# Optimization experiments

Measured on AMD Instinct MI355X. Metric: run time of the kernel, lower is better.

Reference implementation:

```python
import jax, jax.numpy as jnp
import numpy as np

D_MODEL = 1024
N_HEADS = 16
HEAD_DIM = D_MODEL // N_HEADS
THETA = 10000.0


def _rope_tables(seq_len, d_k, dtype):
    pos = jnp.arange(seq_len, dtype=jnp.float32)
    dim = jnp.arange(0, d_k, 2, dtype=jnp.float32)
    inv_freq = 1.0 / (THETA ** (dim / d_k))  # [d_k//2]
    angle = pos[:, None] * inv_freq[None, :]  # [seq, d_k//2]
    return jnp.cos(angle).astype(dtype), jnp.sin(angle).astype(dtype)


def _apply_rope(x, cos, sin):
    # x: [B, H, S, d_k]; cos/sin: [S, d_k//2] (interleaved-pair rotation)
    x1 = x[..., ::2]
    x2 = x[..., 1::2]
    r1 = x1 * cos - x2 * sin
    r2 = x1 * sin + x2 * cos
    out = jnp.stack([r1, r2], axis=-1)  # [..., d_k//2, 2]
    return out.reshape(x.shape)


def setup_inputs() -> dict:
    key = jax.random.key(0)
    ks = jax.random.split(key, 5)
    B, S, D = 4, 2048, D_MODEL
    std = np.sqrt(2.0 / (D + D)).astype(np.float32)
    x = jax.random.normal(ks[0], (B, S, D), dtype=jnp.float32)
    wq = jax.random.normal(ks[1], (D, D), dtype=jnp.float32) * std
    wk = jax.random.normal(ks[2], (D, D), dtype=jnp.float32) * std
    wv = jax.random.normal(ks[3], (D, D), dtype=jnp.float32) * std
    wo = jax.random.normal(ks[4], (D, D), dtype=jnp.float32) * std
    return {"x": x, "wq": wq, "wk": wk, "wv": wv, "wo": wo}


def reference(x, wq, wk, wv, wo):
    B, S, D = x.shape
    H, dk = N_HEADS, HEAD_DIM
    # projections (weight stored [d_out, d_in])
    q = jnp.einsum('oi,bsi->bso', wq, x)
    k = jnp.einsum('oi,bsi->bso', wk, x)
    v = jnp.einsum('oi,bsi->bso', wv, x)
    # split heads -> [B, H, S, dk]
    q = q.reshape(B, S, H, dk).transpose(0, 2, 1, 3)
    k = k.reshape(B, S, H, dk).transpose(0, 2, 1, 3)
    v = v.reshape(B, S, H, dk).transpose(0, 2, 1, 3)
    cos, sin = _rope_tables(S, dk, x.dtype)
    q = _apply_rope(q, cos, sin)
    k = _apply_rope(k, cos, sin)
    scale = 1.0 / np.sqrt(dk)
    logits = jnp.einsum('bhqd,bhkd->bhqk', q, k) * scale
    causal = jnp.tril(jnp.ones((S, S), dtype=bool))
    logits = jnp.where(causal, logits, -jnp.inf)
    probs = jax.nn.softmax(logits, axis=-1)
    ctx = jnp.einsum('bhqk,bhkd->bhqd', probs, v)
    ctx = ctx.transpose(0, 2, 1, 3).reshape(B, S, D)
    return jnp.einsum('oi,bsi->bso', wo, ctx)
```

## Files before the change

### kernel.cpp

```cpp
#include <hip/hip_runtime.h>
#include <hip/hip_bf16.h>
#include <cstdint>
#include <cstddef>


typedef __bf16 bf16;
typedef __bf16 bf16x2 __attribute__((ext_vector_type(2)));
typedef __bf16 bf16x4 __attribute__((ext_vector_type(4)));
typedef __bf16 bf16x8 __attribute__((ext_vector_type(8)));
typedef float  f32x4  __attribute__((ext_vector_type(4)));

#define SEQ 2048
#define NH  16
#define DM  1024
#define MFMA16 __builtin_amdgcn_mfma_f32_16x16x32_bf16

__device__ __forceinline__ void async16(bf16* lds, const bf16* g) {
  __builtin_amdgcn_global_load_lds(
      (__attribute__((address_space(1))) void*)(g),
      (__attribute__((address_space(3))) void*)(lds), 16, 0, 0);
}

__global__ void cvt_all(const float* __restrict__ x,
                        const float* __restrict__ w0, const float* __restrict__ w1,
                        const float* __restrict__ w2, const float* __restrict__ w3,
                        bf16* __restrict__ xb, bf16* __restrict__ wb) {
  int i = blockIdx.x * blockDim.x + threadIdx.x;
  float4 f;
  bf16x4* dst;
  if (i < 2097152) {
    f = ((const float4*)x)[i];
    dst = (bf16x4*)xb + i;
  } else {
    int k = i - 2097152;
    int sel = k >> 18, j = k & 262143;
    const float* src = sel == 0 ? w0 : sel == 1 ? w1 : sel == 2 ? w2 : w3;
    f = ((const float4*)src)[j];
    dst = (bf16x4*)wb + k;
  }
  bf16x4 o;
  o.x = (bf16)f.x; o.y = (bf16)f.y; o.z = (bf16)f.z; o.w = (bf16)f.w;
  *dst = o;
}


__global__ void __launch_bounds__(256)
gemm_out(const bf16* __restrict__ A, const bf16* __restrict__ B,
         float* __restrict__ C, int M, int N, int K) {
  __shared__ bf16 As[2][128 * 32];
  __shared__ bf16 Bs[2][128 * 32];
  const int tid  = threadIdx.x;
  const int lane = tid & 63;
  const int w    = tid >> 6;
  const int l15  = lane & 15, g = lane >> 4;
  const int wr   = w >> 1, wc = w & 1;
  const long bm = (long)blockIdx.x * 128, bn = (long)blockIdx.y * 128;

  f32x4 acc[4][4] = {};

  const int r0 = tid >> 2;
  const int c0 = (tid & 3) << 3;
  const bf16* aB = A + (bm + r0) * K + c0;
  const bf16* bB = B + (bn + r0) * K + c0;

  async16(&As[0][(size_t)tid * 8],        aB);
  async16(&As[0][2048 + (size_t)tid * 8], aB + (size_t)64 * K);
  async16(&Bs[0][(size_t)tid * 8],        bB);
  async16(&Bs[0][2048 + (size_t)tid * 8], bB + (size_t)64 * K);

  const int nkt = K >> 5;
  for (int kt = 0; kt < nkt; ++kt) {
    const int cur = kt & 1, nxt = cur ^ 1;
    __syncthreads();
    if (kt + 1 < nkt) {
      const bf16* ap = aB + (kt + 1) * 32;
      const bf16* bp = bB + (kt + 1) * 32;
      async16(&As[nxt][(size_t)tid * 8],        ap);
      async16(&As[nxt][2048 + (size_t)tid * 8], ap + (size_t)64 * K);
      async16(&Bs[nxt][(size_t)tid * 8],        bp);
      async16(&Bs[nxt][2048 + (size_t)tid * 8], bp + (size_t)64 * K);
    }
    bf16x8 af[4], bfr[4];
#pragma unroll
    for (int mf = 0; mf < 4; ++mf)
      af[mf] = *(const bf16x8*)&As[cur][(wr * 64 + mf * 16 + l15) * 32 + g * 8];
#pragma unroll
    for (int nf = 0; nf < 4; ++nf)
      bfr[nf] = *(const bf16x8*)&Bs[cur][(wc * 64 + nf * 16 + l15) * 32 + g * 8];
#pragma unroll
    for (int mf = 0; mf < 4; ++mf)
#pragma unroll
      for (int nf = 0; nf < 4; ++nf)
        acc[mf][nf] = MFMA16(af[mf], bfr[nf], acc[mf][nf], 0, 0, 0);
  }

#pragma unroll
  for (int mf = 0; mf < 4; ++mf)
#pragma unroll
    for (int nf = 0; nf < 4; ++nf)
#pragma unroll
      for (int r = 0; r < 4; ++r) {
        long m = bm + wr * 64 + mf * 16 + g * 4 + r;
        long n = bn + wc * 64 + nf * 16 + l15;
        C[m * N + n] = acc[mf][nf][r];
      }
}

__global__ void __launch_bounds__(256)
gemm_qkv(const bf16* __restrict__ A, const bf16* __restrict__ Wqkv,
         bf16* __restrict__ Qo, bf16* __restrict__ Ko, bf16* __restrict__ Vto,
         int M, int K) {
  __shared__ bf16 As[2][128 * 32];
  __shared__ bf16 Bs[2][128 * 32];
  const int tid  = threadIdx.x;
  const int lane = tid & 63;
  const int w    = tid >> 6;
  const int l15  = lane & 15, g = lane >> 4;
  const int wr   = w >> 1, wc = w & 1;
  const long bm  = (long)blockIdx.x * 128;
  const long bnG = (long)blockIdx.y * 128;
  const int region = blockIdx.y >> 3;
  const long bn  = (long)(blockIdx.y & 7) * 128;

  f32x4 acc[4][4] = {};

  const int r0 = tid >> 2;
  const int c0 = (tid & 3) << 3;
  const bf16* aB = A + (bm + r0) * K + c0;
  const bf16* bB = Wqkv + (bnG + r0) * K + c0;

  async16(&As[0][(size_t)tid * 8],        aB);
  async16(&As[0][2048 + (size_t)tid * 8], aB + (size_t)64 * K);
  async16(&Bs[0][(size_t)tid * 8],        bB);
  async16(&Bs[0][2048 + (size_t)tid * 8], bB + (size_t)64 * K);

  const int nkt = K >> 5;
  for (int kt = 0; kt < nkt; ++kt) {
    const int cur = kt & 1, nxt = cur ^ 1;
    __syncthreads();
    if (kt + 1 < nkt) {
      const bf16* ap = aB + (kt + 1) * 32;
      const bf16* bp = bB + (kt + 1) * 32;
      async16(&As[nxt][(size_t)tid * 8],        ap);
      async16(&As[nxt][2048 + (size_t)tid * 8], ap + (size_t)64 * K);
      async16(&Bs[nxt][(size_t)tid * 8],        bp);
      async16(&Bs[nxt][2048 + (size_t)tid * 8], bp + (size_t)64 * K);
    }
    bf16x8 af[4], bfr[4];
#pragma unroll
    for (int mf = 0; mf < 4; ++mf)
      af[mf] = *(const bf16x8*)&As[cur][(wr * 64 + mf * 16 + l15) * 32 + g * 8];
#pragma unroll
    for (int nf = 0; nf < 4; ++nf)
      bfr[nf] = *(const bf16x8*)&Bs[cur][(wc * 64 + nf * 16 + l15) * 32 + g * 8];
#pragma unroll
    for (int mf = 0; mf < 4; ++mf)
#pragma unroll
      for (int nf = 0; nf < 4; ++nf)
        acc[mf][nf] = MFMA16(af[mf], bfr[nf], acc[mf][nf], 0, 0, 0);
  }

  if (region < 2) {
    bf16* C = region ? Ko : Qo;
    const float qscale = region ? 1.0f : 0.125f;
#pragma unroll
    for (int nf = 0; nf < 4; ++nf) {
      const int d = nf * 16 + l15;
      const float inv = __expf((float)(d >> 1) * -0.2878231366242558f);
#pragma unroll
      for (int mf = 0; mf < 4; ++mf)
#pragma unroll
        for (int r = 0; r < 4; ++r) {
          long m = bm + wr * 64 + mf * 16 + g * 4 + r;
          long n = bn + wc * 64 + nf * 16 + l15;
          float ang = (float)(int)(m & 2047) * inv;
          float sn, cn;
          __sincosf(ang, &sn, &cn);
          float mine  = acc[mf][nf][r];
          float other = __shfl_xor(mine, 1);
          float res = (d & 1) ? (other * sn + mine * cn)
                              : (mine * cn - other * sn);
          C[m * DM + n] = (bf16)(res * qscale);
        }
    }
  } else {
#pragma unroll
    for (int mf = 0; mf < 4; ++mf)
#pragma unroll
      for (int nf = 0; nf < 4; ++nf) {
        long s0 = bm + wr * 64 + mf * 16 + g * 4;
        long b  = s0 >> 11;
        long s  = s0 & 2047;
        long n  = bn + wc * 64 + nf * 16 + l15;
        long h  = n >> 6, d = n & 63;
        bf16x4 v;
#pragma unroll
        for (int r = 0; r < 4; ++r) v[r] = (bf16)acc[mf][nf][r];
        *(bf16x4*)&Vto[(((b * NH + h) * 64 + d) << 11) + s] = v;
      }
  }
}

__global__ void __launch_bounds__(256, 2)
attn_kernel(const bf16* __restrict__ Q, const bf16* __restrict__ Kg,
            const bf16* __restrict__ Vt, bf16* __restrict__ ctx) {
  __shared__ bf16 Ks[2][64 * 64];
  __shared__ bf16 Vs[2][64 * 64];
  __shared__ bf16 Ps[4 * 2048];
  const int tid  = threadIdx.x;
  const int lane = tid & 63, w = tid >> 6;
  const int l15  = lane & 15, g = lane >> 4;
  const int bid  = (int)blockIdx.x;
  const int qts  = 15 - (bid >> 6);
  const int bh   = bid & 63;
  const int b  = bh >> 4, h = bh & 15;
  const int qw = qts * 128 + w * 32;
  const int ktmax = 2 * qts + 1;

  bf16x8 qf[2][2];
#pragma unroll
  for (int qg = 0; qg < 2; ++qg) {
    const bf16* qp = Q + ((size_t)(b * SEQ + qw + qg * 16 + l15)) * DM + h * 64 + g * 8;
    qf[qg][0] = *(const bf16x8*)qp;
    qf[qg][1] = *(const bf16x8*)(qp + 32);
  }

  f32x4 o[2][4] = {};
  float l_run[2] = {0.f, 0.f};

  const int srow = tid >> 3, scc = tid & 7;
  const int swc  = 8 * (scc ^ (srow & 7));
  const bf16* kb0 = Kg + ((size_t)(b * SEQ + srow)) * DM + h * 64 + swc;
  const bf16* vb0 = Vt + ((size_t)(bh * 64 + srow)) * SEQ + swc;
  bf16* Pw = &Ps[w * 2048];

  async16(&Ks[0][(size_t)tid * 8],        kb0);
  async16(&Ks[0][2048 + (size_t)tid * 8], kb0 + (size_t)32 * DM);
  async16(&Vs[0][(size_t)tid * 8],        vb0);
  async16(&Vs[0][2048 + (size_t)tid * 8], vb0 + (size_t)32 * SEQ);

  for (int kt = 0; kt <= ktmax; ++kt) {
    const int kv0 = kt * 64;
    const int cur = kt & 1, nxt = cur ^ 1;
    __syncthreads();
    if (kt < ktmax) {
      const bf16* kp = kb0 + (size_t)(kt + 1) * 64 * DM;
      const bf16* vp = vb0 + (size_t)(kt + 1) * 64;
      async16(&Ks[nxt][(size_t)tid * 8],        kp);
      async16(&Ks[nxt][2048 + (size_t)tid * 8], kp + (size_t)32 * DM);
      async16(&Vs[nxt][(size_t)tid * 8],        vp);
      async16(&Vs[nxt][2048 + (size_t)tid * 8], vp + (size_t)32 * SEQ);
    }

    if (kv0 > qw + 31) continue;

    f32x4 sa[2][4] = {};
    __builtin_amdgcn_s_setprio(1);
#pragma unroll
    for (int kk = 0; kk < 2; ++kk)
#pragma unroll
      for (int mf = 0; mf < 4; ++mf) {
        const int row = mf * 16 + l15;
        bf16x8 kf = *(const bf16x8*)&Ks[cur][row * 64 + 8 * ((kk * 4 + g) ^ (row & 7))];
        sa[0][mf] = MFMA16(kf, qf[0][kk], sa[0][mf], 0, 0, 0);
        sa[1][mf] = MFMA16(kf, qf[1][kk], sa[1][mf], 0, 0, 0);
      }
    __builtin_amdgcn_s_setprio(0);

#pragma unroll
    for (int j = 0; j < 2; ++j) {
      const int qg = j;
      float p[16];
#pragma unroll
      for (int mf = 0; mf < 4; ++mf)
#pragma unroll
        for (int r = 0; r < 4; ++r) p[mf * 4 + r] = sa[j][mf][r];
      if (kv0 + 63 > qw + qg * 16) {
        const int qidx = qw + qg * 16 + l15;
#pragma unroll
        for (int mf = 0; mf < 4; ++mf)
#pragma unroll
          for (int r = 0; r < 4; ++r)
            if (kv0 + mf * 16 + g * 4 + r > qidx) p[mf * 4 + r] = -1e30f;
      }
      float ts = 0.f;
#pragma unroll
      for (int i = 0; i < 16; ++i) { p[i] = __expf(p[i] - 8.0f); ts += p[i]; }
      l_run[qg] += ts;
#pragma unroll
      for (int mf = 0; mf < 4; ++mf) {
        bf16x4 pv;
#pragma unroll
        for (int r = 0; r < 4; ++r) pv[r] = (bf16)p[mf * 4 + r];
        const int cc = mf * 2 + (g >> 1);
        *(bf16x4*)&Pw[j * 1024 + l15 * 64 + 8 * (cc ^ (l15 & 7)) + (g & 1) * 4] = pv;
      }
    }

    __builtin_amdgcn_s_setprio(1);
#pragma unroll
    for (int kk = 0; kk < 2; ++kk) {
      const int pc = 8 * ((kk * 4 + g) ^ (l15 & 7));
      bf16x8 pa0 = *(const bf16x8*)&Pw[l15 * 64 + pc];
      bf16x8 pa1 = *(const bf16x8*)&Pw[1024 + l15 * 64 + pc];
#pragma unroll
      for (int nf = 0; nf < 4; ++nf) {
        const int vrow = nf * 16 + l15;
        bf16x8 vf = *(const bf16x8*)&Vs[cur][vrow * 64 + 8 * ((kk * 4 + g) ^ (vrow & 7))];
        o[0][nf] = MFMA16(pa0, vf, o[0][nf], 0, 0, 0);
        o[1][nf] = MFMA16(pa1, vf, o[1][nf], 0, 0, 0);
      }
    }
    __builtin_amdgcn_s_setprio(0);
  }

#pragma unroll
  for (int qg = 0; qg < 2; ++qg) {
    float ts = l_run[qg];
    ts += __shfl_xor(ts, 16);
    ts += __shfl_xor(ts, 32);
    float lr[4];
#pragma unroll
    for (int r = 0; r < 4; ++r) lr[r] = 1.0f / __shfl(ts, g * 4 + r);
#pragma unroll
    for (int nf = 0; nf < 4; ++nf)
#pragma unroll
      for (int r = 0; r < 4; ++r) {
        size_t off = ((size_t)(b * SEQ + qw + qg * 16 + g * 4 + r)) * DM + h * 64 + nf * 16 + l15;
        ctx[off] = (bf16)(o[qg][nf][r] * lr[r]);
      }
  }
}

extern "C" void kernel_launch(void* const* d_in, const int* in_sizes, int n_in,
                              void* d_out, int out_size, void* d_ws, size_t ws_size,
                              hipStream_t stream) {
  const float* x  = (const float*)d_in[0];
  const float* wq = (const float*)d_in[1];
  const float* wk = (const float*)d_in[2];
  const float* wv = (const float*)d_in[3];
  const float* wo = (const float*)d_in[4];
  float* out = (float*)d_out;
  char* ws = (char*)d_ws;

  bf16* xb  = (bf16*)(ws);
  bf16* Qb  = (bf16*)(ws + ((size_t)16 << 20));
  bf16* Kb  = (bf16*)(ws + ((size_t)32 << 20));
  bf16* Vt  = (bf16*)(ws + ((size_t)48 << 20));
  bf16* wqb = (bf16*)(ws + ((size_t)64 << 20));
  bf16* wob = (bf16*)(ws + ((size_t)70 << 20));

  cvt_all<<<12288, 256, 0, stream>>>(x, wq, wk, wv, wo, xb, wqb);

  gemm_qkv<<<dim3(64, 24), 256, 0, stream>>>(xb, wqb, Qb, Kb, Vt, 8192, 1024);

  attn_kernel<<<1024, 256, 0, stream>>>(Qb, Kb, Vt, xb );

  gemm_out<<<dim3(64, 8), 256, 0, stream>>>(xb, wob, out, 8192, 1024, 1024);
}
```

Before: 171.4 us.

## Move RoPE out of QKV GEMM epilogue into attention Q load and separate K pass

Removes the per-element sincos/shuffle RoPE epilogue from the QKV projection GEMM so Q and K are stored raw. Q rotation and the 1/sqrt(dk) scale are now applied when the attention kernel loads its Q fragments. K rotation runs in a new standalone elementwise kernel with vectorized 8-wide accesses. The aim is a lighter GEMM epilogue, paid for by an extra launch plus a read and write of all of K, and by bf16 rounding before rotation.

```diff
diff --git a/kernel.cpp b/kernel.cpp
--- a/kernel.cpp
+++ b/kernel.cpp
@@ -162,27 +162,16 @@
 
   if (region < 2) {
     bf16* C = region ? Ko : Qo;
-    const float qscale = region ? 1.0f : 0.125f;
-#pragma unroll
-    for (int nf = 0; nf < 4; ++nf) {
-      const int d = nf * 16 + l15;
-      const float inv = __expf((float)(d >> 1) * -0.2878231366242558f);
-#pragma unroll
-      for (int mf = 0; mf < 4; ++mf)
+#pragma unroll
+    for (int mf = 0; mf < 4; ++mf)
+#pragma unroll
+      for (int nf = 0; nf < 4; ++nf)
 #pragma unroll
         for (int r = 0; r < 4; ++r) {
           long m = bm + wr * 64 + mf * 16 + g * 4 + r;
           long n = bn + wc * 64 + nf * 16 + l15;
-          float ang = (float)(int)(m & 2047) * inv;
-          float sn, cn;
-          __sincosf(ang, &sn, &cn);
-          float mine  = acc[mf][nf][r];
-          float other = __shfl_xor(mine, 1);
-          float res = (d & 1) ? (other * sn + mine * cn)
-                              : (mine * cn - other * sn);
-          C[m * DM + n] = (bf16)(res * qscale);
+          C[m * DM + n] = (bf16)acc[mf][nf][r];
         }
-    }
   } else {
 #pragma unroll
     for (int mf = 0; mf < 4; ++mf)
@@ -199,6 +188,26 @@
         *(bf16x4*)&Vto[(((b * NH + h) * 64 + d) << 11) + s] = v;
       }
   }
+}
+
+__global__ void rope_k(bf16* __restrict__ K) {
+  int i = blockIdx.x * blockDim.x + threadIdx.x;
+  size_t e = (size_t)i * 8;
+  const int d0 = (int)(e & 63);
+  const int s  = (int)((e >> 10) & 2047);
+  bf16x8 v = *(bf16x8*)&K[e];
+#pragma unroll
+  for (int t = 0; t < 4; ++t) {
+    const int j = (d0 >> 1) + t;
+    float inv = __expf((float)j * -0.2878231366242558f);
+    float ang = (float)s * inv;
+    float sn, cn;
+    __sincosf(ang, &sn, &cn);
+    float k1 = (float)v[2 * t], k2 = (float)v[2 * t + 1];
+    v[2 * t]     = (bf16)(k1 * cn - k2 * sn);
+    v[2 * t + 1] = (bf16)(k1 * sn + k2 * cn);
+  }
+  *(bf16x8*)&K[e] = v;
 }
 
 __global__ void __launch_bounds__(256, 2)
@@ -220,9 +229,24 @@
   bf16x8 qf[2][2];
 #pragma unroll
   for (int qg = 0; qg < 2; ++qg) {
-    const bf16* qp = Q + ((size_t)(b * SEQ + qw + qg * 16 + l15)) * DM + h * 64 + g * 8;
-    qf[qg][0] = *(const bf16x8*)qp;
-    qf[qg][1] = *(const bf16x8*)(qp + 32);
+    const int srq = qw + qg * 16 + l15;
+    const bf16* qp = Q + ((size_t)(b * SEQ + srq)) * DM + h * 64 + g * 8;
+#pragma unroll
+    for (int kk = 0; kk < 2; ++kk) {
+      bf16x8 v = *(const bf16x8*)(qp + kk * 32);
+#pragma unroll
+      for (int t = 0; t < 4; ++t) {
+        const int j = kk * 16 + g * 4 + t;
+        float inv = __expf((float)j * -0.2878231366242558f);
+        float ang = (float)srq * inv;
+        float sn, cn;
+        __sincosf(ang, &sn, &cn);
+        float q1 = (float)v[2 * t], q2 = (float)v[2 * t + 1];
+        v[2 * t]     = (bf16)((q1 * cn - q2 * sn) * 0.125f);
+        v[2 * t + 1] = (bf16)((q1 * sn + q2 * cn) * 0.125f);
+      }
+      qf[qg][kk] = v;
+    }
   }
 
   f32x4 o[2][4] = {};
@@ -354,6 +378,8 @@
 
   gemm_qkv<<<dim3(64, 24), 256, 0, stream>>>(xb, wqb, Qb, Kb, Vt, 8192, 1024);
 
+  rope_k<<<4096, 256, 0, stream>>>(Kb);
+
   attn_kernel<<<1024, 256, 0, stream>>>(Qb, Kb, Vt, xb );
 
   gemm_out<<<dim3(64, 8), 256, 0, stream>>>(xb, wob, out, 8192, 1024, 1024);
```

Result: faster. 164.7 us, median of 2 (-3.9%).
